# Kernel tuning notes

Measured on AMD Instinct MI355X. Metric: run time of the kernel, lower is better.

## Reference

```python
import jax, jax.numpy as jnp
import numpy as np

N = 50000   # nodes
E = 800000  # edges (avg degree 16)
D = 64      # indim == outdim
H = 64      # hiddim


def setup_inputs() -> dict:
    key = jax.random.key(0)
    ks = jax.random.split(key, 11)

    def w(k, shape):
        return (jax.random.normal(k, shape, jnp.float32) / jnp.sqrt(shape[0])).astype(jnp.float32)

    return {
        "h": jax.random.normal(ks[0], (N, D), jnp.float32),
        "e": jax.random.normal(ks[1], (E, D), jnp.float32),
        "src": jax.random.randint(ks[2], (E,), 0, N, jnp.int32),
        "dst": jax.random.randint(ks[3], (E,), 0, N, jnp.int32),
        # linear_h MLP (bias=False): D -> H -> D
        "Wh1": w(ks[4], (D, H)), "Wh2": w(ks[5], (H, D)),
        # linear_e MLP (bias=False): D -> H -> D
        "We1": w(ks[6], (D, H)), "We2": w(ks[7], (H, D)),
        # proj MLP (bias=True): 3D -> H -> D
        "Wp1": w(ks[8], (3 * D, H)), "bp1": jnp.zeros((H,), jnp.float32),
        "Wp2": w(ks[9], (H, D)), "bp2": jnp.zeros((D,), jnp.float32),
        # attn_linear (bias=False): 3D -> 1
        "Wa": w(ks[10], (3 * D, 1)),
    }


def reference(h, e, src, dst, Wh1, Wh2, We1, We2, Wp1, bp1, Wp2, bp2, Wa):
    relu = jax.nn.relu
    # node / edge feature MLPs (Linear -> ReLU -> Linear, no bias)
    z_h = relu(h @ Wh1) @ Wh2            # [N, D]
    z_e = relu(e @ We1) @ We2            # [E, D]
    # per-edge concat [z_e, z_src, z_dst]
    z = jnp.concatenate([z_e, z_h[src], z_h[dst]], axis=1)  # [E, 3D]
    # edge projection MLP (with bias)
    e_proj = relu(z @ Wp1 + bp1) @ Wp2 + bp2                 # [E, D]
    # attention score + attn activation (ReLU)
    a = relu((z @ Wa)[:, 0])                                  # [E]
    # segment softmax over incoming edges of each destination node
    m = jax.ops.segment_max(a, dst, num_segments=N)
    m = jnp.where(jnp.isfinite(m), m, 0.0)                    # zero-degree nodes
    ex = jnp.exp(a - m[dst])
    s = jax.ops.segment_sum(ex, dst, num_segments=N)
    alpha = ex / jnp.maximum(s[dst], 1e-9)                    # [E]
    # weighted scatter-sum of source features
    h_out = jax.ops.segment_sum(alpha[:, None] * z_h[src], dst, num_segments=N)  # [N, D]
    # final activation (batch_norm=False, dropout=0)
    return relu(h_out), relu(e_proj)
```

## Files before the change

### kernel.cpp

```cpp
#include <hip/hip_runtime.h>
#include <hip/hip_bf16.h>

#define DIM 64
#define BM 128

typedef __attribute__((ext_vector_type(8))) short bf16x8;
typedef __attribute__((ext_vector_type(4))) float f32x4;

__device__ __forceinline__ short f2bf_hw(float x) {
    __hip_bfloat16 b = __float2bfloat16(x);
    return (short)reinterpret_cast<unsigned short&>(b);
}
__device__ __forceinline__ float bf2f_hw(short s) {
    unsigned u = ((unsigned)(unsigned short)s) << 16;
    return __uint_as_float(u);
}
__device__ __forceinline__ void split8(f32x4 a, f32x4 b, bf16x8& hi, bf16x8& lo) {
    float v[8] = {a[0], a[1], a[2], a[3], b[0], b[1], b[2], b[3]};
    #pragma unroll
    for (int i = 0; i < 8; ++i) {
        short h = f2bf_hw(v[i]);
        hi[i] = h;
        lo[i] = f2bf_hw(v[i] - bf2f_hw(h));
    }
}
__device__ __forceinline__ int swz(int row, int colbyte) {
    return row * 256 + (colbyte ^ ((row & 7) << 4));
}

__global__ __launch_bounds__(256) void k_prep_hist(
    const float* __restrict__ We1, const float* __restrict__ We2,
    const float* __restrict__ Wp1, const float* __restrict__ Wp2,
    const float* __restrict__ Wh1, const float* __restrict__ Wh2,
    unsigned short* __restrict__ whi, unsigned short* __restrict__ wlo,
    const int* __restrict__ dst, int* __restrict__ cnt, int E)
{
    int t = blockIdx.x * 256 + threadIdx.x;
    if (t < 32768) {
        int e_ = t & 7, lane = (t >> 3) & 63, frag = (t >> 9) & 7, layer = t >> 12;
        int kt = frag >> 2, nt = frag & 3;
        int k = kt * 32 + ((lane >> 4) * 8) + e_;
        int n = nt * 16 + (lane & 15);
        const float* W;
        switch (layer) {
            case 0: W = We1; break;
            case 1: W = We2; break;
            case 2: W = Wp1; break;
            case 3: W = Wp2; break;
            case 4: W = Wh1; break;
            case 5: W = Wh2; break;
            case 6: W = Wp1 + 64 * 64; break;
            default: W = Wp1 + 128 * 64; break;
        }
        float w = W[k * 64 + n];
        short h = f2bf_hw(w);
        whi[t] = (unsigned short)h;
        wlo[t] = (unsigned short)f2bf_hw(w - bf2f_hw(h));
    }
    for (int i = t; i < E; i += gridDim.x * 256)
        atomicAdd(&cnt[dst[i]], 1);
}

__global__ __launch_bounds__(256) void node_mfma(
    const float* __restrict__ h,
    const unsigned short* __restrict__ whi, const unsigned short* __restrict__ wlo,
    const float* __restrict__ Wa,
    float* __restrict__ z_h, float* __restrict__ u_s, float* __restrict__ u_d,
    float* __restrict__ as_, float* __restrict__ ad_, int N)
{
    __shared__ float act[BM * 64];
    char* lds = (char*)act;
    const int lane  = threadIdx.x & 63;
    const int wave  = threadIdx.x >> 6;
    const int wrow0 = wave * 32;
    const long node0 = (long)blockIdx.x * BM;
    const int g   = lane >> 4;
    const int c15 = lane & 15;

    f32x4 acc[2][4];
    auto zacc = [&]() {
        #pragma unroll
        for (int mt = 0; mt < 2; ++mt)
            #pragma unroll
            for (int nt = 0; nt < 4; ++nt)
                #pragma unroll
                for (int rr = 0; rr < 4; ++rr) acc[mt][nt][rr] = 0.f;
    };

    auto mfma_layer = [&](int layer) {
        #pragma unroll
        for (int kt = 0; kt < 2; ++kt) {
            bf16x8 ah[2], al[2];
            #pragma unroll
            for (int mt = 0; mt < 2; ++mt) {
                f32x4 a0, a1;
                if (layer == 4) {
                    long nr = node0 + wrow0 + mt * 16 + c15; if (nr >= N) nr = N - 1;
                    const f32x4* p = (const f32x4*)(h + nr * 64 + kt * 32 + g * 8);
                    a0 = p[0];
                    a1 = p[1];
                } else {
                    int row = wrow0 + mt * 16 + c15;
                    int cb  = kt * 128 + g * 32;
                    a0 = *(const f32x4*)(lds + swz(row, cb));
                    a1 = *(const f32x4*)(lds + swz(row, cb + 16));
                }
                split8(a0, a1, ah[mt], al[mt]);
            }
            __builtin_amdgcn_s_setprio(1);
            #pragma unroll
            for (int nt = 0; nt < 4; ++nt) {
                int fo = ((layer * 8 + kt * 4 + nt) * 64 + lane) * 8;
                bf16x8 bh = *(const bf16x8*)(whi + fo);
                bf16x8 bl = *(const bf16x8*)(wlo + fo);
                #pragma unroll
                for (int mt = 0; mt < 2; ++mt) {
                    acc[mt][nt] = __builtin_amdgcn_mfma_f32_16x16x32_bf16(ah[mt], bh, acc[mt][nt], 0, 0, 0);
                    acc[mt][nt] = __builtin_amdgcn_mfma_f32_16x16x32_bf16(ah[mt], bl, acc[mt][nt], 0, 0, 0);
                    acc[mt][nt] = __builtin_amdgcn_mfma_f32_16x16x32_bf16(al[mt], bh, acc[mt][nt], 0, 0, 0);
                }
            }
            __builtin_amdgcn_s_setprio(0);
        }
    };

    auto writeback = [&](bool relu) {
        #pragma unroll
        for (int mt = 0; mt < 2; ++mt)
            #pragma unroll
            for (int nt = 0; nt < 4; ++nt)
                #pragma unroll
                for (int rr = 0; rr < 4; ++rr) {
                    int row  = wrow0 + mt * 16 + g * 4 + rr;
                    int colb = (nt * 16 + c15) * 4;
                    float v = acc[mt][nt][rr];
                    if (relu) v = fmaxf(v, 0.f);
                    *(float*)(lds + swz(row, colb)) = v;
                }
    };

    auto store_global = [&](float* __restrict__ out) {
        #pragma unroll
        for (int mt = 0; mt < 2; ++mt)
            #pragma unroll
            for (int nt = 0; nt < 4; ++nt)
                #pragma unroll
                for (int rr = 0; rr < 4; ++rr) {
                    long nr = node0 + wrow0 + mt * 16 + g * 4 + rr; if (nr >= N) nr = N - 1;
                    out[nr * 64 + nt * 16 + c15] = acc[mt][nt][rr];
                }
    };

    zacc(); mfma_layer(4); writeback(true);
    zacc(); mfma_layer(5);

    {
        float was[4], wad[4];
        #pragma unroll
        for (int nt = 0; nt < 4; ++nt) {
            was[nt] = Wa[64  + nt * 16 + c15];
            wad[nt] = Wa[128 + nt * 16 + c15];
        }
        #pragma unroll
        for (int mt = 0; mt < 2; ++mt) {
            float ps[4], pd[4];
            #pragma unroll
            for (int rr = 0; rr < 4; ++rr) {
                ps[rr] = acc[mt][0][rr] * was[0] + acc[mt][1][rr] * was[1]
                       + acc[mt][2][rr] * was[2] + acc[mt][3][rr] * was[3];
                pd[rr] = acc[mt][0][rr] * wad[0] + acc[mt][1][rr] * wad[1]
                       + acc[mt][2][rr] * wad[2] + acc[mt][3][rr] * wad[3];
            }
            #pragma unroll
            for (int off = 1; off < 16; off <<= 1)
                #pragma unroll
                for (int rr = 0; rr < 4; ++rr) {
                    ps[rr] += __shfl_xor(ps[rr], off);
                    pd[rr] += __shfl_xor(pd[rr], off);
                }
            if (c15 == 0) {
                #pragma unroll
                for (int rr = 0; rr < 4; ++rr) {
                    long nr = node0 + wrow0 + mt * 16 + g * 4 + rr; if (nr >= N) nr = N - 1;
                    as_[nr] = ps[rr];
                    ad_[nr] = pd[rr];
                }
            }
        }
    }
    store_global(z_h);
    writeback(false);

    zacc(); mfma_layer(6); store_global(u_s);
    zacc(); mfma_layer(7); store_global(u_d);
}

__global__ __launch_bounds__(256) void edge_mfma(
    const float* __restrict__ e, const int* __restrict__ src, const int* __restrict__ dst,
    const float* __restrict__ u_s, const float* __restrict__ u_d,
    const float* __restrict__ as_, const float* __restrict__ ad_,
    const unsigned short* __restrict__ whi, const unsigned short* __restrict__ wlo,
    const float* __restrict__ Wa, const float* __restrict__ bp1, const float* __restrict__ bp2,
    float* __restrict__ eproj, float* __restrict__ abuf, int E)
{
    __shared__ float act[BM * 64];
    char* lds = (char*)act;
    const int lane  = threadIdx.x & 63;
    const int wave  = threadIdx.x >> 6;
    const int wrow0 = wave * 32;
    const long edge0 = (long)blockIdx.x * BM;
    const int g   = lane >> 4;
    const int c15 = lane & 15;

    f32x4 ea[2][2][2];
    #pragma unroll
    for (int mt = 0; mt < 2; ++mt) {
        long er = edge0 + wrow0 + mt * 16 + c15; if (er >= E) er = E - 1;
        #pragma unroll
        for (int kt = 0; kt < 2; ++kt) {
            const f32x4* p = (const f32x4*)(e + er * 64 + kt * 32 + g * 8);
            ea[mt][kt][0] = __builtin_nontemporal_load(p);
            ea[mt][kt][1] = __builtin_nontemporal_load(p + 1);
        }
    }

    float uv[2][4][4], asv[2][4];
    #pragma unroll
    for (int mt = 0; mt < 2; ++mt)
        #pragma unroll
        for (int rr = 0; rr < 4; ++rr) {
            long er = edge0 + wrow0 + mt * 16 + g * 4 + rr; if (er >= E) er = E - 1;
            int sn = src[er], dn = dst[er];
            const float* us = u_s + (size_t)sn * DIM;
            const float* ud = u_d + (size_t)dn * DIM;
            #pragma unroll
            for (int nt = 0; nt < 4; ++nt)
                uv[mt][nt][rr] = us[nt * 16 + c15] + ud[nt * 16 + c15];
            asv[mt][rr] = as_[sn] + ad_[dn];
        }

    f32x4 acc[2][4];
    auto zacc = [&]() {
        #pragma unroll
        for (int mt = 0; mt < 2; ++mt)
            #pragma unroll
            for (int nt = 0; nt < 4; ++nt)
                #pragma unroll
                for (int rr = 0; rr < 4; ++rr) acc[mt][nt][rr] = 0.f;
    };

    auto mfma_layer = [&](int layer) {
        #pragma unroll
        for (int kt = 0; kt < 2; ++kt) {
            bf16x8 ah[2], al[2];
            #pragma unroll
            for (int mt = 0; mt < 2; ++mt) {
                f32x4 a0, a1;
                if (layer == 0) {
                    a0 = ea[mt][kt][0];
                    a1 = ea[mt][kt][1];
                } else {
                    int row = wrow0 + mt * 16 + c15;
                    int cb  = kt * 128 + g * 32;
                    a0 = *(const f32x4*)(lds + swz(row, cb));
                    a1 = *(const f32x4*)(lds + swz(row, cb + 16));
                }
                split8(a0, a1, ah[mt], al[mt]);
            }
            __builtin_amdgcn_s_setprio(1);
            #pragma unroll
            for (int nt = 0; nt < 4; ++nt) {
                int fo = ((layer * 8 + kt * 4 + nt) * 64 + lane) * 8;
                bf16x8 bh = *(const bf16x8*)(whi + fo);
                bf16x8 bl = *(const bf16x8*)(wlo + fo);
                #pragma unroll
                for (int mt = 0; mt < 2; ++mt) {
                    acc[mt][nt] = __builtin_amdgcn_mfma_f32_16x16x32_bf16(ah[mt], bh, acc[mt][nt], 0, 0, 0);
                    acc[mt][nt] = __builtin_amdgcn_mfma_f32_16x16x32_bf16(ah[mt], bl, acc[mt][nt], 0, 0, 0);
                    acc[mt][nt] = __builtin_amdgcn_mfma_f32_16x16x32_bf16(al[mt], bh, acc[mt][nt], 0, 0, 0);
                }
            }
            __builtin_amdgcn_s_setprio(0);
        }
    };

    auto writeback = [&](bool relu) {
        #pragma unroll
        for (int mt = 0; mt < 2; ++mt)
            #pragma unroll
            for (int nt = 0; nt < 4; ++nt)
                #pragma unroll
                for (int rr = 0; rr < 4; ++rr) {
                    int row  = wrow0 + mt * 16 + g * 4 + rr;
                    int colb = (nt * 16 + c15) * 4;
                    float v = acc[mt][nt][rr];
                    if (relu) v = fmaxf(v, 0.f);
                    *(float*)(lds + swz(row, colb)) = v;
                }
    };

    zacc(); mfma_layer(0); writeback(true);
    zacc(); mfma_layer(1);

    {
        float waf[4];
        #pragma unroll
        for (int nt = 0; nt < 4; ++nt) waf[nt] = Wa[nt * 16 + c15];
        #pragma unroll
        for (int mt = 0; mt < 2; ++mt) {
            float part[4];
            #pragma unroll
            for (int rr = 0; rr < 4; ++rr)
                part[rr] = acc[mt][0][rr] * waf[0] + acc[mt][1][rr] * waf[1]
                         + acc[mt][2][rr] * waf[2] + acc[mt][3][rr] * waf[3];
            #pragma unroll
            for (int off = 1; off < 16; off <<= 1)
                #pragma unroll
                for (int rr = 0; rr < 4; ++rr) part[rr] += __shfl_xor(part[rr], off);
            if (c15 == 0) {
                #pragma unroll
                for (int rr = 0; rr < 4; ++rr) {
                    long er = edge0 + wrow0 + mt * 16 + g * 4 + rr; if (er >= E) er = E - 1;
                    __builtin_nontemporal_store(fmaxf(part[rr] + asv[mt][rr], 0.f), abuf + er);
                }
            }
        }
    }
    writeback(false);

    zacc(); mfma_layer(2);
    {
        float b1f[4];
        #pragma unroll
        for (int nt = 0; nt < 4; ++nt) b1f[nt] = bp1[nt * 16 + c15];
        #pragma unroll
        for (int mt = 0; mt < 2; ++mt)
            #pragma unroll
            for (int nt = 0; nt < 4; ++nt)
                #pragma unroll
                for (int rr = 0; rr < 4; ++rr)
                    acc[mt][nt][rr] += uv[mt][nt][rr] + b1f[nt];
    }
    writeback(true);

    zacc(); mfma_layer(3);
    {
        float b2f[4];
        #pragma unroll
        for (int nt = 0; nt < 4; ++nt) b2f[nt] = bp2[nt * 16 + c15];
        #pragma unroll
        for (int mt = 0; mt < 2; ++mt)
            #pragma unroll
            for (int nt = 0; nt < 4; ++nt)
                #pragma unroll
                for (int rr = 0; rr < 4; ++rr) {
                    long er = edge0 + wrow0 + mt * 16 + g * 4 + rr; if (er >= E) er = E - 1;
                    __builtin_nontemporal_store(fmaxf(acc[mt][nt][rr] + b2f[nt], 0.f),
                                                eproj + er * 64 + nt * 16 + c15);
                }
    }
}

__global__ __launch_bounds__(256) void k_scan1(
    const int* __restrict__ cnt, int* __restrict__ ofs, int* __restrict__ bsum, int N)
{
    __shared__ int sm[256];
    int t = threadIdx.x, i = blockIdx.x * 256 + t;
    int v = (i < N) ? cnt[i] : 0;
    sm[t] = v;
    __syncthreads();
    #pragma unroll
    for (int off = 1; off < 256; off <<= 1) {
        int tmp = (t >= off) ? sm[t - off] : 0;
        __syncthreads();
        sm[t] += tmp;
        __syncthreads();
    }
    if (i < N) ofs[i] = sm[t] - v;
    if (t == 255) bsum[blockIdx.x] = sm[255];
}

__global__ __launch_bounds__(256) void k_scan2(int* __restrict__ bsum, int NB)
{
    __shared__ int sm[256];
    int t = threadIdx.x;
    int v = (t < NB) ? bsum[t] : 0;
    sm[t] = v;
    __syncthreads();
    #pragma unroll
    for (int off = 1; off < 256; off <<= 1) {
        int tmp = (t >= off) ? sm[t - off] : 0;
        __syncthreads();
        sm[t] += tmp;
        __syncthreads();
    }
    if (t < NB) bsum[t] = sm[t] - v;
}

__global__ __launch_bounds__(256) void k_scan3(
    int* __restrict__ ofs, int* __restrict__ cursor,
    const int* __restrict__ bsum, int N)
{
    int i = blockIdx.x * 256 + threadIdx.x;
    if (i < N) {
        int o = ofs[i] + bsum[blockIdx.x];
        ofs[i] = o;
        cursor[i] = o;
    }
}

__global__ __launch_bounds__(256) void k_fill(
    const int* __restrict__ dst, const int* __restrict__ src,
    int* __restrict__ cursor, int2* __restrict__ esrc, int E)
{
    int i = blockIdx.x * 256 + threadIdx.x;
    if (i < E) {
        int p = atomicAdd(&cursor[dst[i]], 1);
        esrc[p] = make_int2(i, src[i]);
    }
}

__global__ __launch_bounds__(256) void k_aggregate(
    const float* __restrict__ abuf, const int2* __restrict__ esrc,
    const int* __restrict__ ofs, const int* __restrict__ cnt,
    const float* __restrict__ z_h, float* __restrict__ hout, int N)
{
    int wid  = (blockIdx.x * 256 + threadIdx.x) >> 6;
    int lane = threadIdx.x & 63;
    if (wid >= N) return;
    int grp = lane >> 4, c15 = lane & 15;

    int begin = ofs[wid];
    int deg   = cnt[wid];

    float4 acc = make_float4(0.f, 0.f, 0.f, 0.f);
    float inv_s;

    if (deg <= 64) {
        float a = 0.f; int sidx = 0;
        if (lane < deg) {
            int2 es = esrc[begin + lane];
            a    = abuf[es.x];
            sidx = es.y;
        }
        float m = a;
        #pragma unroll
        for (int off = 32; off; off >>= 1) m = fmaxf(m, __shfl_xor(m, off));

        float ex = (lane < deg) ? __expf(a - m) : 0.f;
        float s = ex;
        #pragma unroll
        for (int off = 32; off; off >>= 1) s += __shfl_xor(s, off);
        inv_s = 1.0f / fmaxf(s, 1e-9f);

        int trips = (deg + 3) >> 2;
        for (int i = 0; i < trips; ++i) {
            int k = grp + 4 * i;
            float w  = __shfl(ex,   k & 63);
            int   sk = __shfl(sidx, k & 63);
            if (k < deg) {
                const float4 v = *(const float4*)(z_h + (size_t)sk * DIM + c15 * 4);
                acc.x = fmaf(w, v.x, acc.x);
                acc.y = fmaf(w, v.y, acc.y);
                acc.z = fmaf(w, v.z, acc.z);
                acc.w = fmaf(w, v.w, acc.w);
            }
        }
    } else {
        float m = 0.f;
        for (int k = lane; k < deg; k += 64) m = fmaxf(m, abuf[esrc[begin + k].x]);
        #pragma unroll
        for (int off = 32; off; off >>= 1) m = fmaxf(m, __shfl_xor(m, off));

        float s = 0.f;
        for (int k = lane; k < deg; k += 64) s += __expf(abuf[esrc[begin + k].x] - m);
        #pragma unroll
        for (int off = 32; off; off >>= 1) s += __shfl_xor(s, off);
        inv_s = 1.0f / fmaxf(s, 1e-9f);

        for (int k = grp; k < deg; k += 4) {
            int2 es = esrc[begin + k];
            float w = __expf(abuf[es.x] - m);
            const float4 v = *(const float4*)(z_h + (size_t)es.y * DIM + c15 * 4);
            acc.x = fmaf(w, v.x, acc.x);
            acc.y = fmaf(w, v.y, acc.y);
            acc.z = fmaf(w, v.z, acc.z);
            acc.w = fmaf(w, v.w, acc.w);
        }
    }

    #pragma unroll
    for (int off = 16; off <= 32; off <<= 1) {
        acc.x += __shfl_xor(acc.x, off);
        acc.y += __shfl_xor(acc.y, off);
        acc.z += __shfl_xor(acc.z, off);
        acc.w += __shfl_xor(acc.w, off);
    }
    if (grp == 0) {
        float4 r = make_float4(fmaxf(acc.x * inv_s, 0.f), fmaxf(acc.y * inv_s, 0.f),
                               fmaxf(acc.z * inv_s, 0.f), fmaxf(acc.w * inv_s, 0.f));
        *(float4*)(hout + (size_t)wid * DIM + c15 * 4) = r;
    }
}

extern "C" void kernel_launch(void* const* d_in, const int* in_sizes, int n_in,
                              void* d_out, int out_size, void* d_ws, size_t ws_size,
                              hipStream_t stream)
{
    const float* h   = (const float*)d_in[0];
    const float* e   = (const float*)d_in[1];
    const int*   src = (const int*)d_in[2];
    const int*   dst = (const int*)d_in[3];
    const float* Wh1 = (const float*)d_in[4];
    const float* Wh2 = (const float*)d_in[5];
    const float* We1 = (const float*)d_in[6];
    const float* We2 = (const float*)d_in[7];
    const float* Wp1 = (const float*)d_in[8];
    const float* bp1 = (const float*)d_in[9];
    const float* Wp2 = (const float*)d_in[10];
    const float* bp2 = (const float*)d_in[11];
    const float* Wa  = (const float*)d_in[12];

    const int N = in_sizes[0] / DIM;
    const int E = in_sizes[1] / DIM;

    float* ws   = (float*)d_ws;
    float* z_h  = ws;  ws += (size_t)N * DIM;
    float* u_s  = ws;  ws += (size_t)N * DIM;
    float* u_d  = ws;  ws += (size_t)N * DIM;
    float* as_  = ws;  ws += N;
    float* ad_  = ws;  ws += N;
    float* abuf = ws;  ws += E;
    int* cnt    = (int*)ws;  ws += N;
    int* ofs    = (int*)ws;  ws += N;
    int* cursor = (int*)ws;  ws += N;
    int2* esrc  = (int2*)ws; ws += (size_t)2 * E;
    int* bsum   = (int*)ws;  ws += 256;
    unsigned short* whi = (unsigned short*)ws;  ws += 32768 / 2;
    unsigned short* wlo = (unsigned short*)ws;  ws += 32768 / 2;

    float* hout  = (float*)d_out;
    float* eproj = hout + (size_t)N * DIM;

    const int NB = (N + 255) / 256;

    hipMemsetAsync(cnt, 0, (size_t)N * sizeof(int), stream);

    k_prep_hist<<<(E + 255) / 256, 256, 0, stream>>>(
        We1, We2, Wp1, Wp2, Wh1, Wh2, whi, wlo, dst, cnt, E);

    k_scan1<<<NB, 256, 0, stream>>>(cnt, ofs, bsum, N);
    k_scan2<<<1, 256, 0, stream>>>(bsum, NB);
    k_scan3<<<NB, 256, 0, stream>>>(ofs, cursor, bsum, N);
    k_fill<<<(E + 255) / 256, 256, 0, stream>>>(dst, src, cursor, esrc, E);

    node_mfma<<<(N + BM - 1) / BM, 256, 0, stream>>>(
        h, whi, wlo, Wa, z_h, u_s, u_d, as_, ad_, N);

    edge_mfma<<<(E + BM - 1) / BM, 256, 0, stream>>>(
        e, src, dst, u_s, u_d, as_, ad_, whi, wlo, Wa, bp1, bp2,
        eproj, abuf, E);

    k_aggregate<<<((N * 64) + 255) / 256, 256, 0, stream>>>(
        abuf, esrc, ofs, cnt, z_h, hout, N);
}
```

Before: 343.0 us.

## Store z_h as bf16, scatter attention scores into CSR order, defer gather loads

```diff
diff --git a/kernel.cpp b/kernel.cpp
--- a/kernel.cpp
+++ b/kernel.cpp
@@ -11,9 +11,8 @@
     __hip_bfloat16 b = __float2bfloat16(x);
     return (short)reinterpret_cast<unsigned short&>(b);
 }
-__device__ __forceinline__ float bf2f_hw(short s) {
-    unsigned u = ((unsigned)(unsigned short)s) << 16;
-    return __uint_as_float(u);
+__device__ __forceinline__ float bf2f_hw(unsigned short s) {
+    return __uint_as_float(((unsigned)s) << 16);
 }
 __device__ __forceinline__ void split8(f32x4 a, f32x4 b, bf16x8& hi, bf16x8& lo) {
     float v[8] = {a[0], a[1], a[2], a[3], b[0], b[1], b[2], b[3]};
@@ -21,7 +20,7 @@
     for (int i = 0; i < 8; ++i) {
         short h = f2bf_hw(v[i]);
         hi[i] = h;
-        lo[i] = f2bf_hw(v[i] - bf2f_hw(h));
+        lo[i] = f2bf_hw(v[i] - bf2f_hw((unsigned short)h));
     }
 }
 __device__ __forceinline__ int swz(int row, int colbyte) {
@@ -55,7 +54,7 @@
         float w = W[k * 64 + n];
         short h = f2bf_hw(w);
         whi[t] = (unsigned short)h;
-        wlo[t] = (unsigned short)f2bf_hw(w - bf2f_hw(h));
+        wlo[t] = (unsigned short)f2bf_hw(w - bf2f_hw((unsigned short)h));
     }
     for (int i = t; i < E; i += gridDim.x * 256)
         atomicAdd(&cnt[dst[i]], 1);
@@ -65,7 +64,7 @@
     const float* __restrict__ h,
     const unsigned short* __restrict__ whi, const unsigned short* __restrict__ wlo,
     const float* __restrict__ Wa,
-    float* __restrict__ z_h, float* __restrict__ u_s, float* __restrict__ u_d,
+    unsigned short* __restrict__ z_hb, float* __restrict__ u_s, float* __restrict__ u_d,
     float* __restrict__ as_, float* __restrict__ ad_, int N)
 {
     __shared__ float act[BM * 64];
@@ -188,7 +187,15 @@
             }
         }
     }
-    store_global(z_h);
+    #pragma unroll
+    for (int mt = 0; mt < 2; ++mt)
+        #pragma unroll
+        for (int nt = 0; nt < 4; ++nt)
+            #pragma unroll
+            for (int rr = 0; rr < 4; ++rr) {
+                long nr = node0 + wrow0 + mt * 16 + g * 4 + rr; if (nr >= N) nr = N - 1;
+                z_hb[nr * 64 + nt * 16 + c15] = (unsigned short)f2bf_hw(acc[mt][nt][rr]);
+            }
     writeback(false);
 
     zacc(); mfma_layer(6); store_global(u_s);
@@ -201,6 +208,7 @@
     const float* __restrict__ as_, const float* __restrict__ ad_,
     const unsigned short* __restrict__ whi, const unsigned short* __restrict__ wlo,
     const float* __restrict__ Wa, const float* __restrict__ bp1, const float* __restrict__ bp2,
+    const int* __restrict__ pos,
     float* __restrict__ eproj, float* __restrict__ abuf, int E)
 {
     __shared__ float act[BM * 64];
@@ -224,19 +232,15 @@
         }
     }
 
-    float uv[2][4][4], asv[2][4];
+    int sn[2][4], dn[2][4];
+    float asv[2][4];
     #pragma unroll
     for (int mt = 0; mt < 2; ++mt)
         #pragma unroll
         for (int rr = 0; rr < 4; ++rr) {
             long er = edge0 + wrow0 + mt * 16 + g * 4 + rr; if (er >= E) er = E - 1;
-            int sn = src[er], dn = dst[er];
-            const float* us = u_s + (size_t)sn * DIM;
-            const float* ud = u_d + (size_t)dn * DIM;
-            #pragma unroll
-            for (int nt = 0; nt < 4; ++nt)
-                uv[mt][nt][rr] = us[nt * 16 + c15] + ud[nt * 16 + c15];
-            asv[mt][rr] = as_[sn] + ad_[dn];
+            sn[mt][rr] = src[er]; dn[mt][rr] = dst[er];
+            asv[mt][rr] = as_[sn[mt][rr]] + ad_[dn[mt][rr]];
         }
 
     f32x4 acc[2][4];
@@ -300,6 +304,19 @@
     };
 
     zacc(); mfma_layer(0); writeback(true);
+
+    float uv[2][4][4];
+    #pragma unroll
+    for (int mt = 0; mt < 2; ++mt)
+        #pragma unroll
+        for (int rr = 0; rr < 4; ++rr) {
+            const float* us = u_s + (size_t)sn[mt][rr] * DIM;
+            const float* ud = u_d + (size_t)dn[mt][rr] * DIM;
+            #pragma unroll
+            for (int nt = 0; nt < 4; ++nt)
+                uv[mt][nt][rr] = us[nt * 16 + c15] + ud[nt * 16 + c15];
+        }
+
     zacc(); mfma_layer(1);
 
     {
@@ -320,8 +337,11 @@
             if (c15 == 0) {
                 #pragma unroll
                 for (int rr = 0; rr < 4; ++rr) {
-                    long er = edge0 + wrow0 + mt * 16 + g * 4 + rr; if (er >= E) er = E - 1;
-                    __builtin_nontemporal_store(fmaxf(part[rr] + asv[mt][rr], 0.f), abuf + er);
+                    long er0 = edge0 + wrow0 + mt * 16 + g * 4 + rr;
+                    if (er0 < E) {
+                        int p = pos[er0];
+                        abuf[p] = fmaxf(part[rr] + asv[mt][rr], 0.f);
+                    }
                 }
             }
         }
@@ -411,19 +431,20 @@
 
 __global__ __launch_bounds__(256) void k_fill(
     const int* __restrict__ dst, const int* __restrict__ src,
-    int* __restrict__ cursor, int2* __restrict__ esrc, int E)
+    int* __restrict__ cursor, int* __restrict__ esrc, int* __restrict__ pos, int E)
 {
     int i = blockIdx.x * 256 + threadIdx.x;
     if (i < E) {
         int p = atomicAdd(&cursor[dst[i]], 1);
-        esrc[p] = make_int2(i, src[i]);
+        esrc[p] = src[i];
+        pos[i] = p;
     }
 }
 
 __global__ __launch_bounds__(256) void k_aggregate(
-    const float* __restrict__ abuf, const int2* __restrict__ esrc,
+    const float* __restrict__ abuf, const int* __restrict__ esrc,
     const int* __restrict__ ofs, const int* __restrict__ cnt,
-    const float* __restrict__ z_h, float* __restrict__ hout, int N)
+    const unsigned short* __restrict__ z_hb, float* __restrict__ hout, int N)
 {
     int wid  = (blockIdx.x * 256 + threadIdx.x) >> 6;
     int lane = threadIdx.x & 63;
@@ -439,9 +460,8 @@
     if (deg <= 64) {
         float a = 0.f; int sidx = 0;
         if (lane < deg) {
-            int2 es = esrc[begin + lane];
-            a    = abuf[es.x];
-            sidx = es.y;
+            a    = abuf[begin + lane];
+            sidx = esrc[begin + lane];
         }
         float m = a;
         #pragma unroll
@@ -459,33 +479,33 @@
             float w  = __shfl(ex,   k & 63);
             int   sk = __shfl(sidx, k & 63);
             if (k < deg) {
-                const float4 v = *(const float4*)(z_h + (size_t)sk * DIM + c15 * 4);
-                acc.x = fmaf(w, v.x, acc.x);
-                acc.y = fmaf(w, v.y, acc.y);
-                acc.z = fmaf(w, v.z, acc.z);
-                acc.w = fmaf(w, v.w, acc.w);
+                const ushort4 v = *(const ushort4*)(z_hb + (size_t)sk * DIM + c15 * 4);
+                acc.x = fmaf(w, bf2f_hw(v.x), acc.x);
+                acc.y = fmaf(w, bf2f_hw(v.y), acc.y);
+                acc.z = fmaf(w, bf2f_hw(v.z), acc.z);
+                acc.w = fmaf(w, bf2f_hw(v.w), acc.w);
             }
         }
     } else {
         float m = 0.f;
-        for (int k = lane; k < deg; k += 64) m = fmaxf(m, abuf[esrc[begin + k].x]);
+        for (int k = lane; k < deg; k += 64) m = fmaxf(m, abuf[begin + k]);
         #pragma unroll
         for (int off = 32; off; off >>= 1) m = fmaxf(m, __shfl_xor(m, off));
 
         float s = 0.f;
-        for (int k = lane; k < deg; k += 64) s += __expf(abuf[esrc[begin + k].x] - m);
+        for (int k = lane; k < deg; k += 64) s += __expf(abuf[begin + k] - m);
         #pragma unroll
         for (int off = 32; off; off >>= 1) s += __shfl_xor(s, off);
         inv_s = 1.0f / fmaxf(s, 1e-9f);
 
         for (int k = grp; k < deg; k += 4) {
-            int2 es = esrc[begin + k];
-            float w = __expf(abuf[es.x] - m);
-            const float4 v = *(const float4*)(z_h + (size_t)es.y * DIM + c15 * 4);
-            acc.x = fmaf(w, v.x, acc.x);
-            acc.y = fmaf(w, v.y, acc.y);
-            acc.z = fmaf(w, v.z, acc.z);
-            acc.w = fmaf(w, v.w, acc.w);
+            float w = __expf(abuf[begin + k] - m);
+            int  sk = esrc[begin + k];
+            const ushort4 v = *(const ushort4*)(z_hb + (size_t)sk * DIM + c15 * 4);
+            acc.x = fmaf(w, bf2f_hw(v.x), acc.x);
+            acc.y = fmaf(w, bf2f_hw(v.y), acc.y);
+            acc.z = fmaf(w, bf2f_hw(v.z), acc.z);
+            acc.w = fmaf(w, bf2f_hw(v.w), acc.w);
         }
     }
 
@@ -525,7 +545,7 @@
     const int E = in_sizes[1] / DIM;
 
     float* ws   = (float*)d_ws;
-    float* z_h  = ws;  ws += (size_t)N * DIM;
+    unsigned short* z_hb = (unsigned short*)ws;  ws += (size_t)N * DIM / 2;
     float* u_s  = ws;  ws += (size_t)N * DIM;
     float* u_d  = ws;  ws += (size_t)N * DIM;
     float* as_  = ws;  ws += N;
@@ -534,7 +554,8 @@
     int* cnt    = (int*)ws;  ws += N;
     int* ofs    = (int*)ws;  ws += N;
     int* cursor = (int*)ws;  ws += N;
-    int2* esrc  = (int2*)ws; ws += (size_t)2 * E;
+    int* esrc   = (int*)ws;  ws += E;
+    int* pos    = (int*)ws;  ws += E;
     int* bsum   = (int*)ws;  ws += 256;
     unsigned short* whi = (unsigned short*)ws;  ws += 32768 / 2;
     unsigned short* wlo = (unsigned short*)ws;  ws += 32768 / 2;
@@ -552,15 +573,15 @@
     k_scan1<<<NB, 256, 0, stream>>>(cnt, ofs, bsum, N);
     k_scan2<<<1, 256, 0, stream>>>(bsum, NB);
     k_scan3<<<NB, 256, 0, stream>>>(ofs, cursor, bsum, N);
-    k_fill<<<(E + 255) / 256, 256, 0, stream>>>(dst, src, cursor, esrc, E);
+    k_fill<<<(E + 255) / 256, 256, 0, stream>>>(dst, src, cursor, esrc, pos, E);
 
     node_mfma<<<(N + BM - 1) / BM, 256, 0, stream>>>(
-        h, whi, wlo, Wa, z_h, u_s, u_d, as_, ad_, N);
+        h, whi, wlo, Wa, z_hb, u_s, u_d, as_, ad_, N);
 
     edge_mfma<<<(E + BM - 1) / BM, 256, 0, stream>>>(
-        e, src, dst, u_s, u_d, as_, ad_, whi, wlo, Wa, bp1, bp2,
+        e, src, dst, u_s, u_d, as_, ad_, whi, wlo, Wa, bp1, bp2, pos,
         eproj, abuf, E);
 
     k_aggregate<<<((N * 64) + 255) / 256, 256, 0, stream>>>(
-        abuf, esrc, ofs, cnt, z_h, hout, N);
-}
+        abuf, esrc, ofs, cnt, z_hb, hout, N);
+}
```

Measured after the change: 367.7 us. 7.2% more time.
